# Kernel optimization log

Hardware: AMD Instinct MI355X
Metric: run time of the kernel (lower is better)

The kernel has to match this reference:

```python
import jax, jax.numpy as jnp
import numpy as np

B, N, D, L = 64, 2047, 512, 4
T = D + 1        # token_dim = d + 1
H = 512          # hidden_dim
LN_EPS = 1e-5
ATTN_EPS = 1e-6


def setup_inputs() -> dict:
    key = jax.random.key(0)
    ks = jax.random.split(key, 10)
    s = 0.01  # matches xavier_uniform_ gain=0.01 small-init magnitude
    return dict(
        xs=jax.random.normal(ks[0], (B, N, D), jnp.float32),
        ys=jax.random.normal(ks[1], (B, N), jnp.float32),
        query_x=jax.random.normal(ks[2], (B, 1, D), jnp.float32),
        Wq=jax.random.normal(ks[3], (L, H, T), jnp.float32) * s,
        Wk=jax.random.normal(ks[4], (L, H, T), jnp.float32) * s,
        Wv=jax.random.normal(ks[5], (L, T, T), jnp.float32) * s,
        Wo=jax.random.normal(ks[6], (L, T, T), jnp.float32) * s,
        ln1_w=jnp.ones((L, T), jnp.float32),
        ln1_b=jnp.zeros((L, T), jnp.float32),
        ln2_w=jnp.ones((L, T), jnp.float32),
        ln2_b=jnp.zeros((L, T), jnp.float32),
        scale=jnp.ones((L,), jnp.float32),
        pred_w=jax.random.normal(ks[7], (1, T), jnp.float32) * 0.02,
    )


def _ln(x, w, b):
    m = jnp.mean(x, axis=-1, keepdims=True)
    v = jnp.var(x, axis=-1, keepdims=True)
    return (x - m) * jax.lax.rsqrt(v + LN_EPS) * w + b


def _l2norm(x):
    n = jnp.sqrt(jnp.sum(x * x, axis=-1, keepdims=True))
    return x / jnp.maximum(n, 1e-12)


def _forward(xs, ys, query_x, Wq, Wk, Wv, Wo, ln1_w, ln1_b, ln2_w, ln2_b, scale, pred_w):
    b = xs.shape[0]
    train_tokens = jnp.concatenate([xs, ys[..., None]], axis=-1)          # [B,N,T]
    query_token = jnp.concatenate([query_x, jnp.zeros((b, 1, 1), xs.dtype)], axis=-1)
    tokens = jnp.concatenate([train_tokens, query_token], axis=1)          # [B,N+1,T]

    def step(tok, p):
        wq, wk, wv, wo, w1, b1, w2, b2, sc = p
        x = _ln(tok, w1, b1)
        Q = jnp.einsum('bnt,ht->bnh', x, wq)
        K = jnp.einsum('bnt,ht->bnh', x, wk)
        V = jnp.einsum('bnt,ut->bnu', x, wv)
        Q = _l2norm(Q)
        K = _l2norm(K)
        s = jax.nn.softplus(sc)
        Qp = (jax.nn.elu(Q) + 1.0) * s
        Kp = jax.nn.elu(K) + 1.0
        KV = jnp.einsum('bnh,bnu->bhu', Kp, V)      # [B,H,T]
        Ksum = jnp.sum(Kp, axis=1)                  # [B,H]
        denom = jnp.einsum('bnh,bh->bn', Qp, Ksum)  # [B,N+1]
        attn = jnp.einsum('bnh,bhu->bnu', Qp, KV) / (denom[..., None] + ATTN_EPS)
        out = jnp.einsum('bnu,tu->bnt', attn, wo) * 0.1 + tok
        return _ln(out, w2, b2), None

    tokens, _ = jax.lax.scan(step, tokens, (Wq, Wk, Wv, Wo, ln1_w, ln1_b, ln2_w, ln2_b, scale))
    q_out = tokens[:, -1, :]                        # [B,T]
    return jnp.einsum('bt,ot->bo', q_out, pred_w)[..., 0]  # [B]


def reference(xs, ys, query_x, Wq, Wk, Wv, Wo, ln1_w, ln1_b, ln2_w, ln2_b, scale, pred_w):
    return _forward(xs, ys, query_x, Wq, Wk, Wv, Wo, ln1_w, ln1_b, ln2_w, ln2_b, scale, pred_w)
```

## Files before the change

### kernel.cpp

```cpp
#include <hip/hip_runtime.h>
#include <cstdint>
#include <cstddef>


typedef unsigned short u16;
typedef float f32x4 __attribute__((ext_vector_type(4)));
typedef unsigned short u16x8 __attribute__((ext_vector_type(8)));

#define P 576
#define NQK 1664
#define VTROWS 514
#define KVLD 640

__device__ __forceinline__ float bf2f(u16 s) {
    union { unsigned u; float f; } v; v.u = ((unsigned)s) << 16; return v.f;
}
__device__ __forceinline__ u16 f2bf(float f) {
    union { float f; unsigned u; } v; v.f = f;
    unsigned r = v.u + 0x7FFF + ((v.u >> 16) & 1);
    return (u16)(r >> 16);
}
__device__ __forceinline__ float wredsum(float v) {
#pragma unroll
    for (int o = 32; o > 0; o >>= 1) v += __shfl_xor(v, o, 64);
    return v;
}
__device__ __forceinline__ f32x4 mfma_16x16x32_bf16(u16x8 a, u16x8 b, f32x4 c) {
    asm volatile("v_mfma_f32_16x16x32_bf16 %0, %1, %2, %0"
                 : "+v"(c) : "v"(a), "v"(b));
    return c;
}
__device__ __forceinline__ void gload_lds16(const u16* g, u16* l) {
    __builtin_amdgcn_global_load_lds(
        (const __attribute__((address_space(1))) void*)g,
        (__attribute__((address_space(3))) void*)l, 16, 0, 0);
}

__global__ __launch_bounds__(256) void k_build_tokens(
    const float* __restrict__ xs, const float* __restrict__ ys,
    const float* __restrict__ qx, u16* __restrict__ tok,
    float* __restrict__ meanb, float* __restrict__ rstdb)
{
    long row = (long)blockIdx.x * 4 + (threadIdx.x >> 6);
    int lane = threadIdx.x & 63;
    int b = (int)(row >> 11), n = (int)(row & 2047);
    const float* src = (n < 2047) ? xs + ((long)(b * 2047 + n)) * 512
                                  : qx + (long)b * 512;
    float4 f0 = *(const float4*)(src + lane * 8);
    float4 f1 = *(const float4*)(src + lane * 8 + 4);
    float y = (n < 2047) ? ys[(long)b * 2047 + n] : 0.f;
    float v[8] = {f0.x, f0.y, f0.z, f0.w, f1.x, f1.y, f1.z, f1.w};
    float s = 0.f, sq = 0.f;
#pragma unroll
    for (int j = 0; j < 8; j++) { s += v[j]; sq += v[j] * v[j]; }
    if (lane == 0) { s += y; sq += y * y; }
    s = wredsum(s); sq = wredsum(sq);
    u16x8 o;
#pragma unroll
    for (int j = 0; j < 8; j++) o[j] = f2bf(v[j]);
    *(u16x8*)(tok + row * P + lane * 8) = o;
    if (lane < 8) {
        u16x8 z8 = {0,0,0,0,0,0,0,0};
        if (lane == 0) z8[0] = f2bf(y);
        *(u16x8*)(tok + row * P + 512 + lane * 8) = z8;
    }
    if (lane == 0) {
        float m = s * (1.f / 513.f);
        float var = sq * (1.f / 513.f) - m * m;
        meanb[row] = m;
        rstdb[row] = 1.f / sqrtf(var + 1e-5f);
    }
}

__global__ __launch_bounds__(256) void k_prep_wcat(
    const float* __restrict__ wq, const float* __restrict__ wk,
    const float* __restrict__ wv, const float* __restrict__ ln1w,
    u16* __restrict__ wcat)
{
    long idx = (long)blockIdx.x * 256 + threadIdx.x;
    if (idx >= 4L * NQK * P) return;
    int t = (int)(idx % P);
    long rem = idx / P;
    int r = (int)(rem % NQK);
    int l = (int)(rem / NQK);
    float v = 0.f;
    if (t < 513) {
        float wsc = ln1w[l * 513 + t];
        if (r < 512)       v = wq[((long)l * 512 + r) * 513 + t] * wsc;
        else if (r < 1024) v = wk[((long)l * 512 + (r - 512)) * 513 + t] * wsc;
        else if (r < 1537) v = wv[((long)l * 513 + (r - 1024)) * 513 + t] * wsc;
    }
    wcat[idx] = f2bf(v);
}

__global__ __launch_bounds__(256) void k_prep_wo(
    const float* __restrict__ wo, u16* __restrict__ wop)
{
    long idx = (long)blockIdx.x * 256 + threadIdx.x;
    if (idx >= 4L * P * P) return;
    int u = (int)(idx % P);
    long rem = idx / P;
    int t = (int)(rem % P);
    int l = (int)(rem / P);
    float v = (t < 513 && u < 513) ? wo[((long)l * 513 + t) * 513 + u] : 0.f;
    wop[idx] = f2bf(v);
}

__global__ __launch_bounds__(256) void k_prep_sums(
    const float* __restrict__ wq, const float* __restrict__ wk,
    const float* __restrict__ wv, const float* __restrict__ ln1w,
    const float* __restrict__ ln1b, float* __restrict__ s1, float* __restrict__ s2)
{
    int id = blockIdx.x * 4 + (threadIdx.x >> 6);
    int lane = threadIdx.x & 63;
    int l = id / NQK, r = id % NQK;
    float a1 = 0.f, a2 = 0.f;
    for (int t = lane; t < 513; t += 64) {
        float wc = 0.f;
        if (r < 512)       wc = wq[((long)l * 512 + r) * 513 + t];
        else if (r < 1024) wc = wk[((long)l * 512 + (r - 512)) * 513 + t];
        else if (r < 1537) wc = wv[((long)l * 513 + (r - 1024)) * 513 + t];
        a1 += ln1w[l * 513 + t] * wc;
        a2 += ln1b[l * 513 + t] * wc;
    }
    a1 = wredsum(a1); a2 = wredsum(a2);
    if (lane == 0) { s1[id] = a1; s2[id] = a2; }
}

__global__ __launch_bounds__(256) void k_ln2(
    const u16* __restrict__ z, u16* __restrict__ tok,
    const float* __restrict__ w, const float* __restrict__ bia,
    float* __restrict__ meanb, float* __restrict__ rstdb)
{
    long row = (long)blockIdx.x * 4 + (threadIdx.x >> 6);
    int lane = threadIdx.x & 63;
    const u16* zp = z + row * P;
    u16* tp = tok + row * P;
    u16x8 a0 = *(const u16x8*)(zp + lane * 8);
    u16x8 a1 = {0,0,0,0,0,0,0,0};
    if (lane < 8) a1 = *(const u16x8*)(zp + 512 + lane * 8);
    float v0[8], v1[8];
#pragma unroll
    for (int j = 0; j < 8; j++) v0[j] = bf2f(a0[j]);
#pragma unroll
    for (int j = 0; j < 8; j++) v1[j] = (lane < 8) ? bf2f(a1[j]) : 0.f;
    float s = 0.f, sq = 0.f;
#pragma unroll
    for (int j = 0; j < 8; j++) { s += v0[j]; sq += v0[j] * v0[j]; }
#pragma unroll
    for (int j = 0; j < 8; j++) { s += v1[j]; sq += v1[j] * v1[j]; }
    s = wredsum(s); sq = wredsum(sq);
    float mean = s * (1.f / 513.f);
    float var = sq * (1.f / 513.f) - mean * mean;
    float rstd = 1.f / sqrtf(var + 1e-5f);
    float so = 0.f, so2 = 0.f;
    u16x8 o0;
    float of0[8];
#pragma unroll
    for (int j = 0; j < 8; j++) {
        int t = lane * 8 + j;
        of0[j] = (v0[j] - mean) * rstd * w[t] + bia[t];
        so += of0[j]; so2 += of0[j] * of0[j];
        o0[j] = f2bf(of0[j]);
    }
    float of1[8];
#pragma unroll
    for (int j = 0; j < 8; j++) {
        int t = 512 + lane * 8 + j;
        float ov = 0.f;
        if (lane < 8 && t < 513) ov = (v1[j] - mean) * rstd * w[t] + bia[t];
        of1[j] = ov;
        so += ov; so2 += ov * ov;
    }
    so = wredsum(so); so2 = wredsum(so2);
    *(u16x8*)(tp + lane * 8) = o0;
    if (lane < 8) {
        u16x8 o1;
#pragma unroll
        for (int j = 0; j < 8; j++) o1[j] = f2bf(of1[j]);
        *(u16x8*)(tp + 512 + lane * 8) = o1;
    }
    if (lane == 0) {
        float m2 = so * (1.f / 513.f);
        float v2 = so2 * (1.f / 513.f) - m2 * m2;
        meanb[row] = m2;
        rstdb[row] = 1.f / sqrtf(v2 + 1e-5f);
    }
}

__global__ __launch_bounds__(256) void k_qkt(
    u16* __restrict__ qkv, u16* __restrict__ kpt,
    float* __restrict__ ksum, const float* __restrict__ scale, int l)
{
    long row0 = (long)blockIdx.x * 64;
    int b = (int)(row0 >> 11);
    int nloc = (int)(row0 & 2047);
    int tid = threadIdx.x, lane = tid & 63, w = tid >> 6;
    float s = log1pf(expf(scale[l]));
    __shared__ u16 Kp[64][520];
    __shared__ u16 T2[64 * 80];

#pragma unroll 4
    for (int i = 0; i < 16; i++) {
        int rl = w * 16 + i;
        u16* rp = qkv + (row0 + rl) * NQK;
        u16x8 q8 = *(const u16x8*)(rp + lane * 8);
        u16x8 k8 = *(const u16x8*)(rp + 512 + lane * 8);
        float qf[8], kf[8];
        float sq = 0.f, sk = 0.f;
#pragma unroll
        for (int j = 0; j < 8; j++) { qf[j] = bf2f(q8[j]); sq += qf[j] * qf[j]; }
#pragma unroll
        for (int j = 0; j < 8; j++) { kf[j] = bf2f(k8[j]); sk += kf[j] * kf[j]; }
        sq = wredsum(sq); sk = wredsum(sk);
        float rnq = 1.f / fmaxf(sqrtf(sq), 1e-12f);
        float rnk = 1.f / fmaxf(sqrtf(sk), 1e-12f);
        u16x8 o, kk;
#pragma unroll
        for (int j = 0; j < 8; j++) {
            float q = qf[j] * rnq;
            float qp = (q > 0.f) ? (q + 1.f) : expf(q);
            o[j] = f2bf(qp * s);
            float kv = kf[j] * rnk;
            kv = (kv > 0.f) ? (kv + 1.f) : expf(kv);
            kk[j] = f2bf(kv);
        }
        *(u16x8*)(rp + lane * 8) = o;
        *(u16x8*)&Kp[rl][lane * 8] = kk;
    }
    __syncthreads();

    int r = tid >> 2;
    int c0 = (tid & 3) * 16;
    for (int ct = 0; ct < 8; ct++) {
        u16x8 a = *(const u16x8*)&Kp[r][ct * 64 + c0];
        u16x8 d = *(const u16x8*)&Kp[r][ct * 64 + c0 + 8];
#pragma unroll
        for (int j = 0; j < 8; j++) T2[(c0 + j) * 80 + r] = a[j];
#pragma unroll
        for (int j = 0; j < 8; j++) T2[(c0 + 8 + j) * 80 + r] = d[j];
        __syncthreads();
        u16x8 w0 = *(const u16x8*)&T2[r * 80 + c0];
        u16x8 w1 = *(const u16x8*)&T2[r * 80 + c0 + 8];
        u16* dst = kpt + ((long)(b * 512 + ct * 64 + r)) * 2048 + nloc + c0;
        *(u16x8*)dst = w0;
        *(u16x8*)(dst + 8) = w1;
        float part = 0.f;
#pragma unroll
        for (int j = 0; j < 8; j++) part += bf2f(w0[j]) + bf2f(w1[j]);
        part += __shfl_xor(part, 1, 64);
        part += __shfl_xor(part, 2, 64);
        if ((tid & 3) == 0)
            atomicAdd(&ksum[(long)b * 512 + ct * 64 + r], part);
        __syncthreads();
    }
}

__global__ __launch_bounds__(256) void k_denom(
    const u16* __restrict__ qkv, const float* __restrict__ ksum,
    float* __restrict__ denom)
{
    long row = (long)blockIdx.x * 4 + (threadIdx.x >> 6);
    int lane = threadIdx.x & 63;
    int b = (int)(row >> 11);
    u16x8 q = *(const u16x8*)(qkv + row * NQK + lane * 8);
    const float* ks = ksum + (long)b * 512 + lane * 8;
    float acc = 0.f;
#pragma unroll
    for (int j = 0; j < 8; j++) acc += bf2f(q[j]) * ks[j];
    acc = wredsum(acc);
    if (lane == 0) denom[row] = acc;
}

__global__ void k_predict(const u16* __restrict__ tok, const float* __restrict__ pw,
                          float* __restrict__ out)
{
    int b = blockIdx.x;
    int lane = threadIdx.x;
    const u16* rp = tok + ((long)b * 2048 + 2047) * P;
    float acc = 0.f;
    for (int t = lane; t < 513; t += 64) acc += bf2f(rp[t]) * pw[t];
    acc = wredsum(acc);
    if (lane == 0) out[b] = acc;
}

__global__ __launch_bounds__(256) void k_gemm_bt(
    const u16* __restrict__ A, const u16* __restrict__ Bt, u16* __restrict__ C,
    int M, int N, int K, int lda, int ldb, int ldc,
    long sA, long sB, long sC,
    const float* __restrict__ aux1, const float* __restrict__ aux2,
    const float* __restrict__ aux3, const float* __restrict__ aux4,
    long sAux, const u16* __restrict__ Res,
    float cscale, int mode, int r1, int padw,
    int ntm, int ntn, int nbz,
    u16* __restrict__ VT, int vtbase)
{
    int G = ntm * ntn * nbz;
    int id = blockIdx.x;
    int lin = (id & 7) * (G >> 3) + (id >> 3);
    int per = ntm * ntn;
    int bz = lin / per;
    int rem = lin - bz * per;
    int mt = rem / ntn;
    int nt = rem - mt * ntn;
    int m0 = mt * 128, n0 = nt * 128;

    A += (long)bz * sA; Bt += (long)bz * sB; C += (long)bz * sC;
    int tid = threadIdx.x, lane = tid & 63, w = tid >> 6;
    int wr = w >> 1, wc = w & 1;
    __shared__ u16 ldsbuf[2 * 128 * 64];
    u16* Als = ldsbuf;
    u16* Bls = ldsbuf + 128 * 64;
    __shared__ float auxR0[128], auxR1[128], auxA1[128];
    __shared__ float auxC0[128], auxC1[128], auxB1[128];

    if (tid < 128) {
        int gr = m0 + tid; if (gr >= M) gr = M - 1;
        float r0v = cscale, r1v = 0.f, a1v = 0.f;
        if (mode == 1) {
            const float* d1 = aux1 + (long)bz * sAux;
            r0v = cscale / (d1[gr] + 1e-6f);
        } else if (mode == 3) { r0v = aux1[gr]; r1v = aux2[gr]; }
        if (r1) a1v = bf2f(A[(long)gr * lda + K]);
        auxR0[tid] = r0v; auxR1[tid] = r1v; auxA1[tid] = a1v;
    } else {
        int t = tid - 128;
        int gc = n0 + t; if (gc >= N) gc = N - 1;
        float c0v = 0.f, c1v = 0.f, b1v = 0.f;
        if (mode == 3) { c0v = aux3[gc]; c1v = aux4[gc]; }
        if (r1) b1v = bf2f(Bt[(long)gc * ldb + K]);
        auxC0[t] = c0v; auxC1[t] = c1v; auxB1[t] = b1v;
    }

    f32x4 acc[4][4];
#pragma unroll
    for (int m = 0; m < 4; m++)
#pragma unroll
        for (int n = 0; n < 4; n++) { acc[m][n][0]=0.f; acc[m][n][1]=0.f; acc[m][n][2]=0.f; acc[m][n][3]=0.f; }

    int srow = lane >> 3;
    int scol = (lane & 7) * 8;
    int scolsw = scol ^ (srow << 3);
    int swz = (lane & 7) << 3;

    for (int k0 = 0; k0 < K; k0 += 64) {
#pragma unroll
        for (int i = 0; i < 4; i++) {
            int rt = (w * 4 + i) * 8 + srow;
            int gr = m0 + rt; gr = (gr < M) ? gr : (M - 1);
            gload_lds16(A + (long)gr * lda + k0 + scolsw, &Als[(w * 4 + i) * 512]);
        }
#pragma unroll
        for (int i = 0; i < 4; i++) {
            int rt = (w * 4 + i) * 8 + srow;
            int gc = n0 + rt; gc = (gc < N) ? gc : (N - 1);
            gload_lds16(Bt + (long)gc * ldb + k0 + scolsw, &Bls[(w * 4 + i) * 512]);
        }
        __syncthreads();
#pragma unroll
        for (int ks = 0; ks < 2; ks++) {
            u16x8 af[4], bfv[4];
#pragma unroll
            for (int m = 0; m < 4; m++) {
                int row = wr * 64 + m * 16 + (lane & 15);
                af[m] = *(const u16x8*)&Als[row * 64 + ((ks * 32 + (lane >> 4) * 8) ^ swz)];
            }
#pragma unroll
            for (int n = 0; n < 4; n++) {
                int col = wc * 64 + n * 16 + (lane & 15);
                bfv[n] = *(const u16x8*)&Bls[col * 64 + ((ks * 32 + (lane >> 4) * 8) ^ swz)];
            }
#pragma unroll
            for (int m = 0; m < 4; m++)
#pragma unroll
                for (int n = 0; n < 4; n++)
                    acc[m][n] = mfma_16x16x32_bf16(af[m], bfv[n], acc[m][n]);
        }
        __syncthreads();
    }

    bool isvt = (VT != nullptr) && (n0 >= vtbase);

    if (Res) {
        const u16* Rp = Res + (long)bz * sC;
#pragma unroll
        for (int i = 0; i < 8; i++) {
            int lrow = i * 16 + (tid >> 4);
            int lcol = (tid & 15) * 8;
            long gr = m0 + lrow; if (gr > (long)M - 1) gr = M - 1;
            long gcol = (long)n0 + lcol;
            long mx = (long)ldc - 8; if (gcol > mx) gcol = mx;
            *(u16x8*)&ldsbuf[lrow * 128 + lcol] = *(const u16x8*)&Rp[gr * ldc + gcol];
        }
        __syncthreads();
    }

    asm volatile("s_nop 7\n\ts_nop 7" ::: );

    if (!isvt) {
#pragma unroll
        for (int m = 0; m < 4; m++) {
            int lrbase = wr * 64 + m * 16 + ((lane >> 4) << 2);
#pragma unroll
            for (int n = 0; n < 4; n++) {
                int lc = wc * 64 + n * 16 + (lane & 15);
                float c0v = auxC0[lc], c1v = auxC1[lc], b1v = auxB1[lc];
#pragma unroll
                for (int r = 0; r < 4; r++) {
                    int lr = lrbase + r;
                    float wv = acc[m][n][r] + auxA1[lr] * b1v;
                    float v;
                    if (mode == 3) v = auxR1[lr] * (wv - auxR0[lr] * c0v) + c1v;
                    else {
                        v = wv * auxR0[lr];
                        if (Res) v += bf2f(ldsbuf[lr * 128 + lc]);
                    }
                    ldsbuf[lr * 128 + lc] = f2bf(v);
                }
            }
        }
        __syncthreads();

        int lcol = (tid & 15) * 8;
        int gc0 = n0 + lcol;
        bool colok = padw || (gc0 + 8 <= N);
#pragma unroll
        for (int i = 0; i < 8; i++) {
            int lrow = i * 16 + (tid >> 4);
            int gr = m0 + lrow;
            if (gr < M && colok) {
                *(u16x8*)&C[(long)gr * ldc + gc0] = *(const u16x8*)&ldsbuf[lrow * 128 + lcol];
            }
        }
    } else {
        int u0 = n0 - vtbase;
        int b = m0 >> 11;
        int nloc = m0 & 2047;
#pragma unroll
        for (int m = 0; m < 4; m++) {
            int lrbase = wr * 64 + m * 16 + ((lane >> 4) << 2);
#pragma unroll
            for (int n = 0; n < 4; n++) {
                int lc = wc * 64 + n * 16 + (lane & 15);
                float c0v = auxC0[lc], c1v = auxC1[lc], b1v = auxB1[lc];
#pragma unroll
                for (int r = 0; r < 4; r++) {
                    int lr = lrbase + r;
                    float wv = acc[m][n][r] + auxA1[lr] * b1v;
                    float v = (mode == 3) ? (auxR1[lr] * (wv - auxR0[lr] * c0v) + c1v)
                                          : (wv * auxR0[lr]);
                    ldsbuf[lc * 128 + (lr ^ ((lc & 7) << 3))] = f2bf(v);
                }
            }
        }
        __syncthreads();

        int nc = (tid & 15) * 8;
        const u16x8 ones = {0x3F80,0x3F80,0x3F80,0x3F80,0x3F80,0x3F80,0x3F80,0x3F80};
#pragma unroll
        for (int i = 0; i < 8; i++) {
            int ur = i * 16 + (tid >> 4);
            int u = u0 + ur;
            if (u < VTROWS) {
                u16x8 vv;
                if (u == 513) vv = ones;
                else vv = *(const u16x8*)&ldsbuf[ur * 128 + (nc ^ ((ur & 7) << 3))];
                *(u16x8*)&VT[((long)b * VTROWS + u) * 2048 + nloc + nc] = vv;
            }
        }
    }
}

extern "C" void kernel_launch(void* const* d_in, const int* in_sizes, int n_in,
                              void* d_out, int out_size, void* d_ws, size_t ws_size,
                              hipStream_t stream)
{
    const float* xs    = (const float*)d_in[0];
    const float* ys    = (const float*)d_in[1];
    const float* qx    = (const float*)d_in[2];
    const float* Wq    = (const float*)d_in[3];
    const float* Wk    = (const float*)d_in[4];
    const float* Wv    = (const float*)d_in[5];
    const float* Wo    = (const float*)d_in[6];
    const float* ln1w  = (const float*)d_in[7];
    const float* ln1b  = (const float*)d_in[8];
    const float* ln2w  = (const float*)d_in[9];
    const float* ln2b  = (const float*)d_in[10];
    const float* scale = (const float*)d_in[11];
    const float* predw = (const float*)d_in[12];
    float* out = (float*)d_out;

    char* ws = (char*)d_ws;
    u16*   tok   = (u16*)(ws + 0L);
    u16*   buf1  = (u16*)(ws + 150994944L);
    u16*   qkv   = (u16*)(ws + 301989888L);
    u16*   kpt   = (u16*)(ws + 738197504L);
    u16*   kvh   = (u16*)(ws + 872415232L);
    float* denom = (float*)(ws + 914358272L);
    float* meanb = (float*)(ws + 914882560L);
    float* rstdb = (float*)(ws + 915406848L);
    float* ksum  = (float*)(ws + 915931136L);
    u16*   wcat  = (u16*)(ws + 916062208L);
    u16*   wop   = (u16*)(ws + 923729920L);
    float* s1    = (float*)(ws + 926384128L);
    float* s2    = (float*)(ws + 926410752L);
    u16*   w2t   = kpt;

    k_build_tokens<<<32768, 256, 0, stream>>>(xs, ys, qx, tok, meanb, rstdb);
    {
        long n1 = 4L * NQK * P;
        k_prep_wcat<<<(int)((n1 + 255) / 256), 256, 0, stream>>>(Wq, Wk, Wv, ln1w, wcat);
        long n2 = 4L * P * P;
        k_prep_wo<<<(int)((n2 + 255) / 256), 256, 0, stream>>>(Wo, wop);
        k_prep_sums<<<1664, 256, 0, stream>>>(Wq, Wk, Wv, ln1w, ln1b, s1, s2);
    }

    for (int l = 0; l < 4; l++) {
        hipMemsetAsync(ksum, 0, 64 * 512 * sizeof(float), stream);
        k_gemm_bt<<<13312, 256, 0, stream>>>(tok, wcat + (long)l * NQK * P, qkv,
            131072, NQK, 512, P, P, NQK, 0, 0, 0,
            meanb, rstdb, s1 + l * NQK, s2 + l * NQK, 0, nullptr,
            1.f, 3, 1, 0, 1024, 13, 1,
            buf1, 1024);
        k_qkt<<<2048, 256, 0, stream>>>(qkv, kpt, ksum, scale, l);
        k_gemm_bt<<<1280, 256, 0, stream>>>(kpt, buf1, kvh,
            512, VTROWS, 2048, 2048, 2048, KVLD,
            512L * 2048, (long)VTROWS * 2048, 512L * KVLD,
            nullptr, nullptr, nullptr, nullptr, 0, nullptr, 1.f, 0, 0, 1,
            4, 5, 64, nullptr, 1 << 30);
        k_denom<<<32768, 256, 0, stream>>>(qkv, ksum, denom);
        k_gemm_bt<<<1280, 256, 0, stream>>>(wop + (long)l * P * P, kvh, w2t,
            576, 512, 512, P, KVLD, 512,
            0, 512L * KVLD, 576L * 512,
            nullptr, nullptr, nullptr, nullptr, 0, nullptr, 1.f, 0, 1, 0,
            5, 4, 64, nullptr, 1 << 30);
        k_gemm_bt<<<5120, 256, 0, stream>>>(qkv, w2t, buf1,
            2048, P, 512, NQK, 512, P,
            2048L * NQK, 576L * 512, 2048L * P,
            denom, nullptr, nullptr, nullptr, 2048, tok,
            0.1f, 1, 0, 0, 16, 5, 64, nullptr, 1 << 30);
        k_ln2<<<32768, 256, 0, stream>>>(buf1, tok, ln2w + l * 513, ln2b + l * 513,
                                         meanb, rstdb);
    }
    k_predict<<<64, 64, 0, stream>>>(tok, predw, out);
}
```

Before: 3.441 ms.

## Fold LN2 and next-layer LN1 algebraically into GEMM epilogues, drop normalized token writes

Replaces the k_ln2 pass, which read the pre-LN residual and wrote normalized tokens, with a statistics-only kernel (k_lnstats). It computes per-row LN2 and subsequent LN1 coefficients in closed form from moment sums. The next layer's QKV GEMM then consumes the un-normalized residual z directly. LN2 gamma is folded into the weights, and the affine corrections are applied in a new epilogue mode using precomputed per-column sums. The residual add reconstructs the normalized previous token on the fly, and the final prediction applies LN2 inline. This removes a full-size token write and read per layer, at the cost of more epilogue arithmetic and numerical risk from computing the variance via expanded sums in bf16-derived values.

New measurement: 3.898 ms. 13.3% more time.

```diff
diff --git a/kernel.cpp b/kernel.cpp
--- a/kernel.cpp
+++ b/kernel.cpp
@@ -75,7 +75,7 @@
 __global__ __launch_bounds__(256) void k_prep_wcat(
     const float* __restrict__ wq, const float* __restrict__ wk,
     const float* __restrict__ wv, const float* __restrict__ ln1w,
-    u16* __restrict__ wcat)
+    const float* __restrict__ ln2w, u16* __restrict__ wcat)
 {
     long idx = (long)blockIdx.x * 256 + threadIdx.x;
     if (idx >= 4L * NQK * P) return;
@@ -86,6 +86,7 @@
     float v = 0.f;
     if (t < 513) {
         float wsc = ln1w[l * 513 + t];
+        if (l > 0) wsc *= ln2w[(l - 1) * 513 + t];
         if (r < 512)       v = wq[((long)l * 512 + r) * 513 + t] * wsc;
         else if (r < 1024) v = wk[((long)l * 512 + (r - 512)) * 513 + t] * wsc;
         else if (r < 1537) v = wv[((long)l * 513 + (r - 1024)) * 513 + t] * wsc;
@@ -109,82 +110,85 @@
 __global__ __launch_bounds__(256) void k_prep_sums(
     const float* __restrict__ wq, const float* __restrict__ wk,
     const float* __restrict__ wv, const float* __restrict__ ln1w,
-    const float* __restrict__ ln1b, float* __restrict__ s1, float* __restrict__ s2)
+    const float* __restrict__ ln1b, const float* __restrict__ ln2w,
+    const float* __restrict__ ln2b, float* __restrict__ xcol4)
 {
     int id = blockIdx.x * 4 + (threadIdx.x >> 6);
     int lane = threadIdx.x & 63;
     int l = id / NQK, r = id % NQK;
-    float a1 = 0.f, a2 = 0.f;
+    float a21 = 0.f, b2g = 0.f, a1 = 0.f, b1 = 0.f;
     for (int t = lane; t < 513; t += 64) {
         float wc = 0.f;
         if (r < 512)       wc = wq[((long)l * 512 + r) * 513 + t];
         else if (r < 1024) wc = wk[((long)l * 512 + (r - 512)) * 513 + t];
         else if (r < 1537) wc = wv[((long)l * 513 + (r - 1024)) * 513 + t];
-        a1 += ln1w[l * 513 + t] * wc;
-        a2 += ln1b[l * 513 + t] * wc;
-    }
-    a1 = wredsum(a1); a2 = wredsum(a2);
-    if (lane == 0) { s1[id] = a1; s2[id] = a2; }
-}
-
-__global__ __launch_bounds__(256) void k_ln2(
-    const u16* __restrict__ z, u16* __restrict__ tok,
-    const float* __restrict__ w, const float* __restrict__ bia,
-    float* __restrict__ meanb, float* __restrict__ rstdb)
+        float g1 = ln1w[l * 513 + t], bb1 = ln1b[l * 513 + t];
+        float g2 = (l > 0) ? ln2w[(l - 1) * 513 + t] : 0.f;
+        float b2 = (l > 0) ? ln2b[(l - 1) * 513 + t] : 0.f;
+        a1  += g1 * wc;
+        b1  += bb1 * wc;
+        a21 += g2 * g1 * wc;
+        b2g += b2 * g1 * wc;
+    }
+    a21 = wredsum(a21); b2g = wredsum(b2g);
+    a1 = wredsum(a1); b1 = wredsum(b1);
+    if (lane == 0) {
+        xcol4[(long)id * 4 + 0] = a21;
+        xcol4[(long)id * 4 + 1] = b2g;
+        xcol4[(long)id * 4 + 2] = a1;
+        xcol4[(long)id * 4 + 3] = b1;
+    }
+}
+
+__global__ __launch_bounds__(256) void k_lnstats(
+    const u16* __restrict__ z, const float* __restrict__ g2,
+    const float* __restrict__ b2, float* __restrict__ st6)
 {
     long row = (long)blockIdx.x * 4 + (threadIdx.x >> 6);
     int lane = threadIdx.x & 63;
-    const u16* zp = z + row * P;
-    u16* tp = tok + row * P;
-    u16x8 a0 = *(const u16x8*)(zp + lane * 8);
-    u16x8 a1 = {0,0,0,0,0,0,0,0};
-    if (lane < 8) a1 = *(const u16x8*)(zp + 512 + lane * 8);
-    float v0[8], v1[8];
-#pragma unroll
-    for (int j = 0; j < 8; j++) v0[j] = bf2f(a0[j]);
-#pragma unroll
-    for (int j = 0; j < 8; j++) v1[j] = (lane < 8) ? bf2f(a1[j]) : 0.f;
-    float s = 0.f, sq = 0.f;
-#pragma unroll
-    for (int j = 0; j < 8; j++) { s += v0[j]; sq += v0[j] * v0[j]; }
-#pragma unroll
-    for (int j = 0; j < 8; j++) { s += v1[j]; sq += v1[j] * v1[j]; }
-    s = wredsum(s); sq = wredsum(sq);
-    float mean = s * (1.f / 513.f);
-    float var = sq * (1.f / 513.f) - mean * mean;
-    float rstd = 1.f / sqrtf(var + 1e-5f);
-    float so = 0.f, so2 = 0.f;
-    u16x8 o0;
-    float of0[8];
+    const u16* zp = z + row * NQK;
+    u16x8 z8 = *(const u16x8*)(zp + lane * 8);
+    float S1 = 0.f, S2 = 0.f, Sg = 0.f, Sg2z2 = 0.f, Sg21 = 0.f, Sbg = 0.f;
+    float cg = 0.f, cb = 0.f, cg2 = 0.f, cbg = 0.f, cb2 = 0.f;
 #pragma unroll
     for (int j = 0; j < 8; j++) {
         int t = lane * 8 + j;
-        of0[j] = (v0[j] - mean) * rstd * w[t] + bia[t];
-        so += of0[j]; so2 += of0[j] * of0[j];
-        o0[j] = f2bf(of0[j]);
-    }
-    float of1[8];
-#pragma unroll
-    for (int j = 0; j < 8; j++) {
-        int t = 512 + lane * 8 + j;
-        float ov = 0.f;
-        if (lane < 8 && t < 513) ov = (v1[j] - mean) * rstd * w[t] + bia[t];
-        of1[j] = ov;
-        so += ov; so2 += ov * ov;
-    }
-    so = wredsum(so); so2 = wredsum(so2);
-    *(u16x8*)(tp + lane * 8) = o0;
-    if (lane < 8) {
-        u16x8 o1;
-#pragma unroll
-        for (int j = 0; j < 8; j++) o1[j] = f2bf(of1[j]);
-        *(u16x8*)(tp + 512 + lane * 8) = o1;
+        float zv = bf2f(z8[j]);
+        float g = g2[t], b = b2[t];
+        S1 += zv; S2 += zv * zv;
+        Sg += g * zv; Sg2z2 += g * g * zv * zv; Sg21 += g * g * zv;
+        Sbg += g * b * zv;
+        cg += g; cb += b; cg2 += g * g; cbg += g * b; cb2 += b * b;
     }
     if (lane == 0) {
-        float m2 = so * (1.f / 513.f);
-        float v2 = so2 * (1.f / 513.f) - m2 * m2;
-        meanb[row] = m2;
-        rstdb[row] = 1.f / sqrtf(v2 + 1e-5f);
+        float zv = bf2f(zp[512]);
+        float g = g2[512], b = b2[512];
+        S1 += zv; S2 += zv * zv;
+        Sg += g * zv; Sg2z2 += g * g * zv * zv; Sg21 += g * g * zv;
+        Sbg += g * b * zv;
+        cg += g; cb += b; cg2 += g * g; cbg += g * b; cb2 += b * b;
+    }
+    S1 = wredsum(S1); S2 = wredsum(S2); Sg = wredsum(Sg);
+    Sg2z2 = wredsum(Sg2z2); Sg21 = wredsum(Sg21); Sbg = wredsum(Sbg);
+    cg = wredsum(cg); cb = wredsum(cb); cg2 = wredsum(cg2);
+    cbg = wredsum(cbg); cb2 = wredsum(cb2);
+    if (lane == 0) {
+        const float rT = 1.f / 513.f;
+        float mu2 = S1 * rT;
+        float var2 = S2 * rT - mu2 * mu2;
+        float r2 = 1.f / sqrtf(var2 + 1e-5f);
+        float mu1 = (r2 * (Sg - mu2 * cg) + cb) * rT;
+        float Q2 = r2 * r2 * (Sg2z2 - 2.f * mu2 * Sg21 + mu2 * mu2 * cg2)
+                 + 2.f * r2 * (Sbg - mu2 * cbg) + cb2;
+        float var1 = Q2 * rT - mu1 * mu1;
+        float r1 = 1.f / sqrtf(var1 + 1e-5f);
+        float* o = st6 + row * 6;
+        o[0] = r1 * r2;
+        o[1] = -r1 * r2 * mu2;
+        o[2] = r1;
+        o[3] = -r1 * mu1;
+        o[4] = mu2 * r2;
+        o[5] = r2;
     }
 }
 
@@ -272,14 +276,21 @@
     if (lane == 0) denom[row] = acc;
 }
 
-__global__ void k_predict(const u16* __restrict__ tok, const float* __restrict__ pw,
-                          float* __restrict__ out)
+__global__ void k_predict(const u16* __restrict__ z, const float* __restrict__ st6,
+                          const float* __restrict__ g2, const float* __restrict__ b2,
+                          const float* __restrict__ pw, float* __restrict__ out)
 {
     int b = blockIdx.x;
     int lane = threadIdx.x;
-    const u16* rp = tok + ((long)b * 2048 + 2047) * P;
+    long row = (long)b * 2048 + 2047;
+    const u16* rp = z + row * NQK;
+    float mu2r2 = st6[row * 6 + 4], r2 = st6[row * 6 + 5];
     float acc = 0.f;
-    for (int t = lane; t < 513; t += 64) acc += bf2f(rp[t]) * pw[t];
+    for (int t = lane; t < 513; t += 64) {
+        float zt = bf2f(rp[t]);
+        float tokv = zt * r2 * g2[t] - mu2r2 * g2[t] + b2[t];
+        acc += tokv * pw[t];
+    }
     acc = wredsum(acc);
     if (lane == 0) out[b] = acc;
 }
@@ -290,7 +301,7 @@
     long sA, long sB, long sC,
     const float* __restrict__ aux1, const float* __restrict__ aux2,
     const float* __restrict__ aux3, const float* __restrict__ aux4,
-    long sAux, const u16* __restrict__ Res,
+    long sAux, const u16* __restrict__ Res, int ldr, long sRes,
     float cscale, int mode, int r1, int padw,
     int ntm, int ntn, int nbz,
     u16* __restrict__ VT, int vtbase)
@@ -311,25 +322,47 @@
     __shared__ u16 ldsbuf[2 * 128 * 64];
     u16* Als = ldsbuf;
     u16* Bls = ldsbuf + 128 * 64;
-    __shared__ float auxR0[128], auxR1[128], auxA1[128];
-    __shared__ float auxC0[128], auxC1[128], auxB1[128];
+    __shared__ float auxR0[128], auxR1[128], auxR2[128], auxR3[128], auxA1[128];
+    __shared__ float auxC0[128], auxC1[128], auxC2[128], auxC3[128], auxB1[128];
 
     if (tid < 128) {
         int gr = m0 + tid; if (gr >= M) gr = M - 1;
-        float r0v = cscale, r1v = 0.f, a1v = 0.f;
-        if (mode == 1) {
+        float r0v = cscale, r1v = 0.f, r2v = 0.f, r3v = 0.f, a1v = 0.f;
+        if (mode == 1 || mode == 5) {
             const float* d1 = aux1 + (long)bz * sAux;
             r0v = cscale / (d1[gr] + 1e-6f);
-        } else if (mode == 3) { r0v = aux1[gr]; r1v = aux2[gr]; }
+        }
+        if (mode == 3) { r0v = aux1[gr]; r1v = aux2[gr]; }
+        if (mode == 4) {
+            r0v = aux1[(long)gr * 6 + 0]; r1v = aux1[(long)gr * 6 + 1];
+            r2v = aux1[(long)gr * 6 + 2]; r3v = aux1[(long)gr * 6 + 3];
+        }
+        if (mode == 5) {
+            long zr = (long)bz * 2048 + gr;
+            r1v = aux2[zr * 6 + 4]; r2v = aux2[zr * 6 + 5];
+        }
         if (r1) a1v = bf2f(A[(long)gr * lda + K]);
-        auxR0[tid] = r0v; auxR1[tid] = r1v; auxA1[tid] = a1v;
+        auxR0[tid] = r0v; auxR1[tid] = r1v; auxR2[tid] = r2v; auxR3[tid] = r3v;
+        auxA1[tid] = a1v;
     } else {
         int t = tid - 128;
         int gc = n0 + t; if (gc >= N) gc = N - 1;
-        float c0v = 0.f, c1v = 0.f, b1v = 0.f;
-        if (mode == 3) { c0v = aux3[gc]; c1v = aux4[gc]; }
+        float c0v = 0.f, c1v = 0.f, c2v = 0.f, c3v = 0.f, b1v = 0.f;
+        if (mode == 3) {
+            c2v = aux3[(long)gc * 4 + 2]; c3v = aux3[(long)gc * 4 + 3];
+        }
+        if (mode == 4) {
+            c0v = aux3[(long)gc * 4 + 0]; c1v = aux3[(long)gc * 4 + 1];
+            c2v = aux3[(long)gc * 4 + 2]; c3v = aux3[(long)gc * 4 + 3];
+        }
+        if (mode == 5) {
+            bool ok = gc < 513;
+            c0v = ok ? aux3[gc] : 0.f;
+            c1v = ok ? aux4[gc] : 0.f;
+        }
         if (r1) b1v = bf2f(Bt[(long)gc * ldb + K]);
-        auxC0[t] = c0v; auxC1[t] = c1v; auxB1[t] = b1v;
+        auxC0[t] = c0v; auxC1[t] = c1v; auxC2[t] = c2v; auxC3[t] = c3v;
+        auxB1[t] = b1v;
     }
 
     f32x4 acc[4][4];
@@ -382,15 +415,15 @@
     bool isvt = (VT != nullptr) && (n0 >= vtbase);
 
     if (Res) {
-        const u16* Rp = Res + (long)bz * sC;
+        const u16* Rp = Res + (long)bz * sRes;
 #pragma unroll
         for (int i = 0; i < 8; i++) {
             int lrow = i * 16 + (tid >> 4);
             int lcol = (tid & 15) * 8;
             long gr = m0 + lrow; if (gr > (long)M - 1) gr = M - 1;
             long gcol = (long)n0 + lcol;
-            long mx = (long)ldc - 8; if (gcol > mx) gcol = mx;
-            *(u16x8*)&ldsbuf[lrow * 128 + lcol] = *(const u16x8*)&Rp[gr * ldc + gcol];
+            long mx = (long)N - 8; if (gcol > mx) gcol = mx;
+            *(u16x8*)&ldsbuf[lrow * 128 + lcol] = *(const u16x8*)&Rp[gr * ldr + gcol];
         }
         __syncthreads();
     }
@@ -404,13 +437,20 @@
 #pragma unroll
             for (int n = 0; n < 4; n++) {
                 int lc = wc * 64 + n * 16 + (lane & 15);
-                float c0v = auxC0[lc], c1v = auxC1[lc], b1v = auxB1[lc];
 #pragma unroll
                 for (int r = 0; r < 4; r++) {
                     int lr = lrbase + r;
-                    float wv = acc[m][n][r] + auxA1[lr] * b1v;
+                    float wv = acc[m][n][r] + auxA1[lr] * auxB1[lc];
                     float v;
-                    if (mode == 3) v = auxR1[lr] * (wv - auxR0[lr] * c0v) + c1v;
+                    if (mode == 3)
+                        v = auxR1[lr] * (wv - auxR0[lr] * auxC2[lc]) + auxC3[lc];
+                    else if (mode == 4)
+                        v = auxR0[lr] * wv + auxR1[lr] * auxC0[lc]
+                          + auxR2[lr] * auxC1[lc] + auxR3[lr] * auxC2[lc] + auxC3[lc];
+                    else if (mode == 5)
+                        v = wv * auxR0[lr]
+                          + bf2f(ldsbuf[lr * 128 + lc]) * auxR2[lr] * auxC0[lc]
+                          - auxR1[lr] * auxC0[lc] + auxC1[lc];
                     else {
                         v = wv * auxR0[lr];
                         if (Res) v += bf2f(ldsbuf[lr * 128 + lc]);
@@ -442,13 +482,18 @@
 #pragma unroll
             for (int n = 0; n < 4; n++) {
                 int lc = wc * 64 + n * 16 + (lane & 15);
-                float c0v = auxC0[lc], c1v = auxC1[lc], b1v = auxB1[lc];
 #pragma unroll
                 for (int r = 0; r < 4; r++) {
                     int lr = lrbase + r;
-                    float wv = acc[m][n][r] + auxA1[lr] * b1v;
-                    float v = (mode == 3) ? (auxR1[lr] * (wv - auxR0[lr] * c0v) + c1v)
-                                          : (wv * auxR0[lr]);
+                    float wv = acc[m][n][r] + auxA1[lr] * auxB1[lc];
+                    float v;
+                    if (mode == 3)
+                        v = auxR1[lr] * (wv - auxR0[lr] * auxC2[lc]) + auxC3[lc];
+                    else if (mode == 4)
+                        v = auxR0[lr] * wv + auxR1[lr] * auxC0[lc]
+                          + auxR2[lr] * auxC1[lc] + auxR3[lr] * auxC2[lc] + auxC3[lc];
+                    else
+                        v = wv * auxR0[lr];
                     ldsbuf[lc * 128 + (lr ^ ((lc & 7) << 3))] = f2bf(v);
                 }
             }
@@ -502,45 +547,64 @@
     float* ksum  = (float*)(ws + 915931136L);
     u16*   wcat  = (u16*)(ws + 916062208L);
     u16*   wop   = (u16*)(ws + 923729920L);
-    float* s1    = (float*)(ws + 926384128L);
-    float* s2    = (float*)(ws + 926410752L);
+    float* st6   = (float*)(ws + 285736960L);
+    float* xcol4 = (float*)(ws + 288882688L);
     u16*   w2t   = kpt;
+    u16*   zbuf  = qkv + 1024;
 
     k_build_tokens<<<32768, 256, 0, stream>>>(xs, ys, qx, tok, meanb, rstdb);
     {
         long n1 = 4L * NQK * P;
-        k_prep_wcat<<<(int)((n1 + 255) / 256), 256, 0, stream>>>(Wq, Wk, Wv, ln1w, wcat);
+        k_prep_wcat<<<(int)((n1 + 255) / 256), 256, 0, stream>>>(Wq, Wk, Wv, ln1w, ln2w, wcat);
         long n2 = 4L * P * P;
         k_prep_wo<<<(int)((n2 + 255) / 256), 256, 0, stream>>>(Wo, wop);
-        k_prep_sums<<<1664, 256, 0, stream>>>(Wq, Wk, Wv, ln1w, ln1b, s1, s2);
+        k_prep_sums<<<1664, 256, 0, stream>>>(Wq, Wk, Wv, ln1w, ln1b, ln2w, ln2b, xcol4);
     }
 
     for (int l = 0; l < 4; l++) {
         hipMemsetAsync(ksum, 0, 64 * 512 * sizeof(float), stream);
-        k_gemm_bt<<<13312, 256, 0, stream>>>(tok, wcat + (long)l * NQK * P, qkv,
-            131072, NQK, 512, P, P, NQK, 0, 0, 0,
-            meanb, rstdb, s1 + l * NQK, s2 + l * NQK, 0, nullptr,
-            1.f, 3, 1, 0, 1024, 13, 1,
-            buf1, 1024);
+        if (l == 0) {
+            k_gemm_bt<<<13312, 256, 0, stream>>>(tok, wcat, qkv,
+                131072, NQK, 512, P, P, NQK, 0, 0, 0,
+                meanb, rstdb, xcol4, nullptr, 0, nullptr, 0, 0,
+                1.f, 3, 1, 0, 1024, 13, 1,
+                buf1, 1024);
+        } else {
+            k_gemm_bt<<<13312, 256, 0, stream>>>(zbuf, wcat + (long)l * NQK * P, qkv,
+                131072, NQK, 512, NQK, P, NQK, 0, 0, 0,
+                st6, nullptr, xcol4 + (long)l * NQK * 4, nullptr, 0, nullptr, 0, 0,
+                1.f, 4, 1, 0, 1024, 13, 1,
+                buf1, 1024);
+        }
         k_qkt<<<2048, 256, 0, stream>>>(qkv, kpt, ksum, scale, l);
         k_gemm_bt<<<1280, 256, 0, stream>>>(kpt, buf1, kvh,
             512, VTROWS, 2048, 2048, 2048, KVLD,
             512L * 2048, (long)VTROWS * 2048, 512L * KVLD,
-            nullptr, nullptr, nullptr, nullptr, 0, nullptr, 1.f, 0, 0, 1,
+            nullptr, nullptr, nullptr, nullptr, 0, nullptr, 0, 0, 1.f, 0, 0, 1,
             4, 5, 64, nullptr, 1 << 30);
         k_denom<<<32768, 256, 0, stream>>>(qkv, ksum, denom);
         k_gemm_bt<<<1280, 256, 0, stream>>>(wop + (long)l * P * P, kvh, w2t,
             576, 512, 512, P, KVLD, 512,
             0, 512L * KVLD, 576L * 512,
-            nullptr, nullptr, nullptr, nullptr, 0, nullptr, 1.f, 0, 1, 0,
+            nullptr, nullptr, nullptr, nullptr, 0, nullptr, 0, 0, 1.f, 0, 1, 0,
             5, 4, 64, nullptr, 1 << 30);
-        k_gemm_bt<<<5120, 256, 0, stream>>>(qkv, w2t, buf1,
-            2048, P, 512, NQK, 512, P,
-            2048L * NQK, 576L * 512, 2048L * P,
-            denom, nullptr, nullptr, nullptr, 2048, tok,
-            0.1f, 1, 0, 0, 16, 5, 64, nullptr, 1 << 30);
-        k_ln2<<<32768, 256, 0, stream>>>(buf1, tok, ln2w + l * 513, ln2b + l * 513,
-                                         meanb, rstdb);
-    }
-    k_predict<<<64, 64, 0, stream>>>(tok, predw, out);
-}
+        if (l == 0) {
+            k_gemm_bt<<<5120, 256, 0, stream>>>(qkv, w2t, zbuf,
+                2048, P, 512, NQK, 512, NQK,
+                2048L * NQK, 576L * 512, 2048L * NQK,
+                denom, nullptr, nullptr, nullptr, 2048, tok, P, 2048L * P,
+                0.1f, 1, 0, 0, 16, 5, 64, nullptr, 1 << 30);
+        } else {
+            k_gemm_bt<<<5120, 256, 0, stream>>>(qkv, w2t, zbuf,
+                2048, P, 512, NQK, 512, NQK,
+                2048L * NQK, 576L * 512, 2048L * NQK,
+                denom, st6, ln2w + (long)(l - 1) * 513, ln2b + (long)(l - 1) * 513,
+                2048, zbuf, NQK, 2048L * NQK,
+                0.1f, 5, 0, 0, 16, 5, 64, nullptr, 1 << 30);
+        }
+        k_lnstats<<<32768, 256, 0, stream>>>(zbuf, ln2w + (long)l * 513,
+                                             ln2b + (long)l * 513, st6);
+    }
+    k_predict<<<64, 64, 0, stream>>>(zbuf, st6, ln2w + 3L * 513, ln2b + 3L * 513,
+                                     predw, out);
+}
```

## Peel the 513th value/output column out of KV and output GEMMs into side reductions

Applied to the files above, without the earlier changes.

The KV and output GEMMs previously covered 514 and 576 columns, so one extra partial tile (the column at index 512) cost a whole tile row of blocks. That column is now computed separately. Its KV entry is accumulated with atomics inside k_qkt, and its output contribution is a dot product in k_denom that is folded into k_ln2. This trims the GEMM grids to 512-wide tiles, at the cost of extra atomics, a small extra kernel and a memset.

After: 3.342 ms (median of 3 runs). 1.03x faster.

```diff
diff --git a/kernel.cpp b/kernel.cpp
--- a/kernel.cpp
+++ b/kernel.cpp
@@ -130,20 +130,23 @@
 __global__ __launch_bounds__(256) void k_ln2(
     const u16* __restrict__ z, u16* __restrict__ tok,
     const float* __restrict__ w, const float* __restrict__ bia,
-    float* __restrict__ meanb, float* __restrict__ rstdb)
+    float* __restrict__ meanb, float* __restrict__ rstdb,
+    const float* __restrict__ znum, const float* __restrict__ denomb)
 {
     long row = (long)blockIdx.x * 4 + (threadIdx.x >> 6);
     int lane = threadIdx.x & 63;
     const u16* zp = z + row * P;
     u16* tp = tok + row * P;
     u16x8 a0 = *(const u16x8*)(zp + lane * 8);
-    u16x8 a1 = {0,0,0,0,0,0,0,0};
-    if (lane < 8) a1 = *(const u16x8*)(zp + 512 + lane * 8);
+    float zc = 0.f;
+    if (lane == 0)
+        zc = 0.1f * znum[row] / (denomb[row] + 1e-6f) + bf2f(tp[512]);
     float v0[8], v1[8];
 #pragma unroll
     for (int j = 0; j < 8; j++) v0[j] = bf2f(a0[j]);
 #pragma unroll
-    for (int j = 0; j < 8; j++) v1[j] = (lane < 8) ? bf2f(a1[j]) : 0.f;
+    for (int j = 0; j < 8; j++) v1[j] = 0.f;
+    v1[0] = zc;
     float s = 0.f, sq = 0.f;
 #pragma unroll
     for (int j = 0; j < 8; j++) { s += v0[j]; sq += v0[j] * v0[j]; }
@@ -190,7 +193,8 @@
 
 __global__ __launch_bounds__(256) void k_qkt(
     u16* __restrict__ qkv, u16* __restrict__ kpt,
-    float* __restrict__ ksum, const float* __restrict__ scale, int l)
+    float* __restrict__ ksum, float* __restrict__ v512sum,
+    const u16* __restrict__ vt, const float* __restrict__ scale, int l)
 {
     long row0 = (long)blockIdx.x * 64;
     int b = (int)(row0 >> 11);
@@ -230,6 +234,13 @@
     }
     __syncthreads();
 
+    const u16* vrow = vt + ((long)b * VTROWS + 512) * 2048 + nloc + (tid & 3) * 16;
+    u16x8 va = *(const u16x8*)vrow;
+    u16x8 vb = *(const u16x8*)(vrow + 8);
+    float vf[16];
+#pragma unroll
+    for (int j = 0; j < 8; j++) { vf[j] = bf2f(va[j]); vf[8 + j] = bf2f(vb[j]); }
+
     int r = tid >> 2;
     int c0 = (tid & 3) * 16;
     for (int ct = 0; ct < 8; ct++) {
@@ -245,31 +256,53 @@
         u16* dst = kpt + ((long)(b * 512 + ct * 64 + r)) * 2048 + nloc + c0;
         *(u16x8*)dst = w0;
         *(u16x8*)(dst + 8) = w1;
-        float part = 0.f;
-#pragma unroll
-        for (int j = 0; j < 8; j++) part += bf2f(w0[j]) + bf2f(w1[j]);
+        float part = 0.f, p2 = 0.f;
+#pragma unroll
+        for (int j = 0; j < 8; j++) {
+            float k0 = bf2f(w0[j]), k1 = bf2f(w1[j]);
+            part += k0 + k1;
+            p2 += k0 * vf[j] + k1 * vf[8 + j];
+        }
         part += __shfl_xor(part, 1, 64);
         part += __shfl_xor(part, 2, 64);
-        if ((tid & 3) == 0)
+        p2 += __shfl_xor(p2, 1, 64);
+        p2 += __shfl_xor(p2, 2, 64);
+        if ((tid & 3) == 0) {
             atomicAdd(&ksum[(long)b * 512 + ct * 64 + r], part);
-        __syncthreads();
-    }
+            atomicAdd(&v512sum[(long)b * 512 + ct * 64 + r], p2);
+        }
+        __syncthreads();
+    }
+}
+
+__global__ __launch_bounds__(512) void k_v512(
+    const float* __restrict__ v512sum, u16* __restrict__ kvh)
+{
+    int b = blockIdx.x, h = threadIdx.x;
+    kvh[((long)b * 512 + h) * KVLD + 512] = f2bf(v512sum[(long)b * 512 + h]);
 }
 
 __global__ __launch_bounds__(256) void k_denom(
     const u16* __restrict__ qkv, const float* __restrict__ ksum,
-    float* __restrict__ denom)
+    const u16* __restrict__ w2t, float* __restrict__ denom,
+    float* __restrict__ znum)
 {
     long row = (long)blockIdx.x * 4 + (threadIdx.x >> 6);
     int lane = threadIdx.x & 63;
     int b = (int)(row >> 11);
     u16x8 q = *(const u16x8*)(qkv + row * NQK + lane * 8);
     const float* ks = ksum + (long)b * 512 + lane * 8;
-    float acc = 0.f;
-#pragma unroll
-    for (int j = 0; j < 8; j++) acc += bf2f(q[j]) * ks[j];
+    u16x8 w8 = *(const u16x8*)(w2t + (long)b * 576 * 512 + 512 * 512 + lane * 8);
+    float acc = 0.f, acc2 = 0.f;
+#pragma unroll
+    for (int j = 0; j < 8; j++) {
+        float qf = bf2f(q[j]);
+        acc += qf * ks[j];
+        acc2 += qf * bf2f(w8[j]);
+    }
     acc = wredsum(acc);
-    if (lane == 0) denom[row] = acc;
+    acc2 = wredsum(acc2);
+    if (lane == 0) { denom[row] = acc; znum[row] = acc2; }
 }
 
 __global__ void k_predict(const u16* __restrict__ tok, const float* __restrict__ pw,
@@ -504,6 +537,8 @@
     u16*   wop   = (u16*)(ws + 923729920L);
     float* s1    = (float*)(ws + 926384128L);
     float* s2    = (float*)(ws + 926410752L);
+    float* v512s = (float*)(ws + 285736960L);
+    float* znum  = (float*)(ws + 285868032L);
     u16*   w2t   = kpt;
 
     k_build_tokens<<<32768, 256, 0, stream>>>(xs, ys, qx, tok, meanb, rstdb);
@@ -517,30 +552,32 @@
 
     for (int l = 0; l < 4; l++) {
         hipMemsetAsync(ksum, 0, 64 * 512 * sizeof(float), stream);
+        hipMemsetAsync(v512s, 0, 64 * 512 * sizeof(float), stream);
         k_gemm_bt<<<13312, 256, 0, stream>>>(tok, wcat + (long)l * NQK * P, qkv,
             131072, NQK, 512, P, P, NQK, 0, 0, 0,
             meanb, rstdb, s1 + l * NQK, s2 + l * NQK, 0, nullptr,
             1.f, 3, 1, 0, 1024, 13, 1,
             buf1, 1024);
-        k_qkt<<<2048, 256, 0, stream>>>(qkv, kpt, ksum, scale, l);
-        k_gemm_bt<<<1280, 256, 0, stream>>>(kpt, buf1, kvh,
-            512, VTROWS, 2048, 2048, 2048, KVLD,
+        k_qkt<<<2048, 256, 0, stream>>>(qkv, kpt, ksum, v512s, buf1, scale, l);
+        k_gemm_bt<<<1024, 256, 0, stream>>>(kpt, buf1, kvh,
+            512, 512, 2048, 2048, 2048, KVLD,
             512L * 2048, (long)VTROWS * 2048, 512L * KVLD,
             nullptr, nullptr, nullptr, nullptr, 0, nullptr, 1.f, 0, 0, 1,
-            4, 5, 64, nullptr, 1 << 30);
-        k_denom<<<32768, 256, 0, stream>>>(qkv, ksum, denom);
+            4, 4, 64, nullptr, 1 << 30);
+        k_v512<<<64, 512, 0, stream>>>(v512s, kvh);
         k_gemm_bt<<<1280, 256, 0, stream>>>(wop + (long)l * P * P, kvh, w2t,
             576, 512, 512, P, KVLD, 512,
             0, 512L * KVLD, 576L * 512,
             nullptr, nullptr, nullptr, nullptr, 0, nullptr, 1.f, 0, 1, 0,
             5, 4, 64, nullptr, 1 << 30);
-        k_gemm_bt<<<5120, 256, 0, stream>>>(qkv, w2t, buf1,
-            2048, P, 512, NQK, 512, P,
+        k_denom<<<32768, 256, 0, stream>>>(qkv, ksum, w2t, denom, znum);
+        k_gemm_bt<<<4096, 256, 0, stream>>>(qkv, w2t, buf1,
+            2048, 512, 512, NQK, 512, P,
             2048L * NQK, 576L * 512, 2048L * P,
             denom, nullptr, nullptr, nullptr, 2048, tok,
-            0.1f, 1, 0, 0, 16, 5, 64, nullptr, 1 << 30);
+            0.1f, 1, 0, 0, 16, 4, 64, nullptr, 1 << 30);
         k_ln2<<<32768, 256, 0, stream>>>(buf1, tok, ln2w + l * 513, ln2b + l * 513,
-                                         meanb, rstdb);
+                                         meanb, rstdb, znum, denom);
     }
     k_predict<<<64, 64, 0, stream>>>(tok, predw, out);
 }
```
